# Kernel tuning notes

Measured on AMD Instinct MI355X. Metric: run time of the kernel, lower is better.

The kernel has to match this reference:

```python
import jax, jax.numpy as jnp
import numpy as np
from jax import lax

N = 50000      # nodes
E = 1600000    # edges
F = 128        # input features
G = 32         # gnn_hidden_dim
H = 50         # lstm hidden_dim
SEQ = 10       # sequence_length


def setup_inputs() -> dict:
    key = jax.random.key(0)
    ks = jax.random.split(key, 12)
    s = 0.05
    return {
        "x": jax.random.normal(ks[0], (N, F), jnp.float32),
        "W_gcn": jax.random.normal(ks[1], (F, G), jnp.float32) * s,
        "b_gcn": jnp.zeros((G,), jnp.float32),
        "w_ih0": jax.random.normal(ks[2], (4 * H, G), jnp.float32) * s,
        "w_hh0": jax.random.normal(ks[3], (4 * H, H), jnp.float32) * s,
        "b_ih0": jnp.zeros((4 * H,), jnp.float32),
        "b_hh0": jnp.zeros((4 * H,), jnp.float32),
        "w_ih1": jax.random.normal(ks[4], (4 * H, H), jnp.float32) * s,
        "w_hh1": jax.random.normal(ks[5], (4 * H, H), jnp.float32) * s,
        "b_ih1": jnp.zeros((4 * H,), jnp.float32),
        "b_hh1": jnp.zeros((4 * H,), jnp.float32),
        "fc_w": jax.random.normal(ks[6], (1, H), jnp.float32) * s,
        "fc_b": jnp.zeros((1,), jnp.float32),
        "edge_index": jax.random.randint(ks[7], (2, E), 0, N, dtype=jnp.int64),
        "seq_len": SEQ,
    }


def gcn_conv(x, edge_index, W, b):
    # PyG GCNConv: add self-loops, symmetric deg^{-1/2} normalization,
    # linear transform, gather-scale-scatter aggregation at target nodes.
    n = x.shape[0]
    loop = jnp.arange(n, dtype=edge_index.dtype)
    src = jnp.concatenate([edge_index[0], loop])  # message sources j
    dst = jnp.concatenate([edge_index[1], loop])  # aggregation targets i
    deg = jax.ops.segment_sum(jnp.ones_like(dst, dtype=x.dtype), dst,
                              num_segments=n)
    dinv = jnp.where(deg > 0, lax.rsqrt(jnp.maximum(deg, 1.0)), 0.0)
    norm = dinv[src] * dinv[dst]                       # [E+N]
    h = x @ W                                          # [N, G]
    msg = h[src] * norm[:, None]                       # gather + scale
    out = jax.ops.segment_sum(msg, dst, num_segments=n)
    return out + b


def lstm_layer(x_proj, w_hh, b_hh):
    # x_proj: [T, B, 4H] precomputed input projections (i,f,g,o gate order).
    T, B, H4 = x_proj.shape
    Hd = H4 // 4
    h0 = jnp.zeros((B, Hd), x_proj.dtype)
    c0 = jnp.zeros((B, Hd), x_proj.dtype)

    def step(carry, xp):
        h, c = carry
        gates = xp + h @ w_hh.T + b_hh
        i, f, g, o = jnp.split(gates, 4, axis=-1)
        i, f, o = jax.nn.sigmoid(i), jax.nn.sigmoid(f), jax.nn.sigmoid(o)
        g = jnp.tanh(g)
        c = f * c + i * g
        h = o * jnp.tanh(c)
        return (h, c), h

    (h, c), ys = lax.scan(step, (h0, c0), x_proj)
    return ys, h


def reference(x, W_gcn, b_gcn, w_ih0, w_hh0, b_ih0, b_hh0,
              w_ih1, w_hh1, b_ih1, b_hh1, fc_w, fc_b,
              edge_index, seq_len):
    gnn_out = gcn_conv(x, edge_index, W_gcn, b_gcn)        # [N, G]
    # lstm_in = gnn_out repeated seq_len times -> input projection is
    # identical per step; compute once and broadcast (same math).
    p0 = gnn_out @ w_ih0.T + b_ih0                         # [N, 4H]
    x_proj0 = jnp.broadcast_to(p0, (seq_len,) + p0.shape)  # [T, N, 4H]
    ys0, _ = lstm_layer(x_proj0, w_hh0, b_hh0)             # [T, N, H]
    x_proj1 = ys0 @ w_ih1.T + b_ih1                        # [T, N, 4H]
    _, hn1 = lstm_layer(x_proj1, w_hh1, b_hh1)             # [N, H]
    return hn1 @ fc_w.T + fc_b                             # [N, 1]
```

## Files before the change

kernel.cpp:

```cpp
#include <hip/hip_runtime.h>
#include <hip/hip_bf16.h>

typedef __attribute__((ext_vector_type(8))) short short8;
typedef __attribute__((ext_vector_type(4))) float f32x4;

#define L2E 1.442695041f
#define SCAN_B 256

__device__ __forceinline__ short f2bf(float f) {
  union { __hip_bfloat16 b; short s; } u;
  u.b = __float2bfloat16(f);
  return u.s;
}

__device__ __forceinline__ float ldh(const float* p, size_t i) { return p[i]; }
__device__ __forceinline__ float ldh(const __hip_bfloat16* p, size_t i) {
  return __bfloat162float(p[i]);
}
__device__ __forceinline__ void sth(float* p, size_t i, float v) { p[i] = v; }
__device__ __forceinline__ void sth(__hip_bfloat16* p, size_t i, float v) {
  p[i] = __float2bfloat16(v);
}

__device__ __forceinline__ short8 load_gfrag(const float* g, size_t base) {
  const float4* gp = (const float4*)(g + base);
  float4 a = gp[0], b = gp[1];
  short8 t;
  t[0]=f2bf(a.x); t[1]=f2bf(a.y); t[2]=f2bf(a.z); t[3]=f2bf(a.w);
  t[4]=f2bf(b.x); t[5]=f2bf(b.y); t[6]=f2bf(b.z); t[7]=f2bf(b.w);
  return t;
}
__device__ __forceinline__ short8 load_gfrag(const __hip_bfloat16* g, size_t base) {
  return *(const short8*)(g + base);
}

#define OFF_WIH0 0
#define OFF_WHH0 13312
#define OFF_WIH1 39936
#define OFF_WHH1 66560
#define OFF_B0   93184
#define OFF_B1   94016
#define OFF_FCW  94848
#define IMG_BYTES 95056

__global__ void k_detect(const int* __restrict__ ei, int* __restrict__ flag) {
  if (threadIdx.x == 0 && blockIdx.x == 0) {
    int odd_nz = 0, even_nz = 0;
    for (int i = 0; i < 128; ++i) {
      odd_nz |= (ei[2 * i + 1] != 0);
      even_nz |= (ei[2 * i] != 0);
    }
    *flag = (even_nz && !odd_nz) ? 1 : 0;
  }
}


__global__ void k_count(const int* __restrict__ ei, int E,
                        const int* __restrict__ flag, int* __restrict__ cnt) {
  int e = blockIdx.x * blockDim.x + threadIdx.x;
  if (e < E) {
    int d = (*flag) ? ei[2 * (E + e)] : ei[E + e];
    atomicAdd(&cnt[d], 1);
  }
}

__global__ void k_dinv(const int* __restrict__ cnt, float* __restrict__ dinv, int N) {
  int i = blockIdx.x * blockDim.x + threadIdx.x;
  if (i < N) dinv[i] = rsqrtf((float)cnt[i] + 1.0f);
}

__global__ __launch_bounds__(256) void k_scanA(const int* __restrict__ cnt,
                                               float* __restrict__ dinv,
                                               int* __restrict__ bsum, int N) {
  __shared__ int red[256];
  int b = blockIdx.x, t = threadIdx.x;
  int chunk = (N + SCAN_B - 1) / SCAN_B;
  int lo = b * chunk, hi = min(lo + chunk, N);
  int s = 0;
  for (int i = lo + t; i < hi; i += 256) {
    int c = cnt[i];
    dinv[i] = rsqrtf((float)c + 1.0f);
    s += c;
  }
  red[t] = s;
  __syncthreads();
  for (int o = 128; o > 0; o >>= 1) {
    if (t < o) red[t] += red[t + o];
    __syncthreads();
  }
  if (t == 0) bsum[b] = red[0];
}

__global__ __launch_bounds__(256) void k_scanB(int* __restrict__ a,
                                               const int* __restrict__ bsum,
                                               int N) {
  __shared__ int sh[256];
  int b = blockIdx.x, t = threadIdx.x;
  int chunk = (N + SCAN_B - 1) / SCAN_B;
  int lo = b * chunk, hi = min(lo + chunk, N);
  sh[t] = bsum[t];
  __syncthreads();
  for (int o = 1; o < 256; o <<= 1) {
    int u = (t >= o) ? sh[t - o] : 0;
    __syncthreads();
    sh[t] += u;
    __syncthreads();
  }
  int carry = (b == 0) ? 0 : sh[b - 1];
  __syncthreads();
  for (int i0 = lo; i0 < hi; i0 += 256) {
    int i = i0 + t;
    int c = (i < hi) ? a[i] : 0;
    sh[t] = c;
    __syncthreads();
    for (int o = 1; o < 256; o <<= 1) {
      int u = (t >= o) ? sh[t - o] : 0;
      __syncthreads();
      sh[t] += u;
      __syncthreads();
    }
    if (i < hi) a[i] = carry + sh[t] - c;
    carry += sh[255];
    __syncthreads();
  }
}

template <typename CT>
__global__ void k_fill(const int* __restrict__ ei, int E,
                       const int* __restrict__ flag,
                       int* __restrict__ rowst, CT* __restrict__ csr,
                       int lo, int hi) {
  int e = blockIdx.x * blockDim.x + threadIdx.x;
  if (e < E) {
    int is64 = *flag;
    int d = is64 ? ei[2 * (E + e)] : ei[E + e];
    if (d >= lo && d < hi) {
      int s = is64 ? ei[2 * e] : ei[e];
      int p = atomicAdd(&rowst[d], 1);
      csr[p] = (CT)s;
    }
  }
}

template <typename HT>
__global__ __launch_bounds__(256) void k_hs(const float* __restrict__ x,
                                            const float* __restrict__ Wg,
                                            const float* __restrict__ dinv,
                                            HT* __restrict__ hs, int N) {
  __shared__ __align__(16) float xt[64][132];
  __shared__ __align__(16) float Wl[128][32];
  int tid = threadIdx.x;
  int nb = blockIdx.x * 64;
  for (int i = tid; i < 4096; i += 256) Wl[i >> 5][i & 31] = Wg[i];
  const float4* xv = (const float4*)x;
  for (int i = tid; i < 2048; i += 256) {
    int r = i >> 5, c = i & 31;
    float4 v = make_float4(0.f, 0.f, 0.f, 0.f);
    if (nb + r < N) v = xv[(size_t)(nb + r) * 32 + c];
    *(float4*)&xt[r][c * 4] = v;
  }
  __syncthreads();
  int nl = tid >> 2, gq = (tid & 3) * 8;
  float a[8];
#pragma unroll
  for (int j = 0; j < 8; ++j) a[j] = 0.f;
  for (int k = 0; k < 128; ++k) {
    float xk = xt[nl][k];
#pragma unroll
    for (int j = 0; j < 8; ++j) a[j] += xk * Wl[k][gq + j];
  }
  int n = nb + nl;
  if (n < N) {
    float d = dinv[n];
#pragma unroll
    for (int j = 0; j < 8; ++j) sth(hs, (size_t)n * 32 + gq + j, a[j] * d);
  }
}

template <typename HT, typename GT, typename CT>
__global__ void k_gather(const CT* __restrict__ csr, const int* __restrict__ rowst,
                         const HT* __restrict__ hs, const float* __restrict__ dinv,
                         const float* __restrict__ bg, GT* __restrict__ gout,
                         int N) {
  int w = (blockIdx.x * blockDim.x + threadIdx.x) >> 6;
  if (w >= N) return;
  int l = threadIdx.x & 63;
  int g = l & 31, j = l >> 5;
  int end = rowst[w];
  int start = (w == 0) ? 0 : rowst[w - 1];
  int deg = end - start;
  int dmax = min(deg, 64);
  int idx = (l < deg) ? (int)csr[start + l] : 0;
  float acc = 0.0f;
#pragma unroll 1
  for (int base = 0; base < 64; base += 16) {
    if (base >= dmax) break;
#pragma unroll
    for (int i = 0; i < 8; ++i) {
      int e = base + 2 * i + j;
      int src = __shfl(idx, e);
      float v = ldh(hs, (size_t)src * 32 + g);
      acc += (e < dmax) ? v : 0.0f;
    }
  }
  for (int k = start + 64 + j; k < end; k += 2)
    acc += ldh(hs, (size_t)csr[k] * 32 + g);
  acc += __shfl_xor(acc, 32);
  if (j == 0) {
    float v = (acc + ldh(hs, (size_t)w * 32 + g)) * dinv[w] + bg[g];
    sth(gout, (size_t)w * 32 + g, v);
  }
}

template <typename HT>
__global__ void k_scatter(const int* __restrict__ ei, int E,
                          const int* __restrict__ flag,
                          const HT* __restrict__ hs, float* __restrict__ gout) {
  long long gid = (long long)blockIdx.x * blockDim.x + threadIdx.x;
  int e = (int)(gid >> 3), part = (int)(gid & 7);
  if (e >= E) return;
  int is64 = *flag;
  int s = is64 ? ei[2 * e] : ei[e];
  int d = is64 ? ei[2 * (E + e)] : ei[E + e];
  int b = part * 4;
  float* gp = gout + (size_t)d * 32 + b;
  size_t hp = (size_t)s * 32 + b;
  atomicAdd(gp + 0, ldh(hs, hp + 0));
  atomicAdd(gp + 1, ldh(hs, hp + 1));
  atomicAdd(gp + 2, ldh(hs, hp + 2));
  atomicAdd(gp + 3, ldh(hs, hp + 3));
}
template <typename HT>
__global__ void k_finish(const HT* __restrict__ hs, const float* __restrict__ dinv,
                         const float* __restrict__ bg, float* __restrict__ gout,
                         int N) {
  int gid = blockIdx.x * blockDim.x + threadIdx.x;
  if (gid < N * 32) {
    int n = gid >> 5, g = gid & 31;
    gout[gid] = (gout[gid] + ldh(hs, (size_t)gid)) * dinv[n] + bg[g];
  }
}

__global__ void k_prep(const float* __restrict__ wih0, const float* __restrict__ whh0,
                       const float* __restrict__ wih1, const float* __restrict__ whh1,
                       const float* __restrict__ bih0, const float* __restrict__ bhh0,
                       const float* __restrict__ bih1, const float* __restrict__ bhh1,
                       const float* __restrict__ fcw, unsigned char* __restrict__ img) {
  int gid = blockIdx.x * blockDim.x + threadIdx.x;
  int nthr = gridDim.x * blockDim.x;
  {
    short* W = (short*)(img + OFF_WIH0);
    for (int i = gid; i < 208 * 32; i += nthr) {
      int row = i >> 5, k = i & 31, u = row >> 2, q = row & 3;
      float sc = (q == 2) ? 2.0f * L2E : -L2E;
      float v = (u < 50) ? wih0[(q * 50 + u) * 32 + k] * sc : 0.0f;
      W[row * 32 + (k ^ ((row & 3) << 3))] = f2bf(v);
    }
  }
  {
    short* W = (short*)(img + OFF_WHH0);
    for (int i = gid; i < 208 * 64; i += nthr) {
      int row = i >> 6, k = i & 63, u = row >> 2, q = row & 3;
      float sc = (q == 2) ? 2.0f * L2E : -L2E;
      float v = (u < 50 && k < 50) ? whh0[(q * 50 + u) * 50 + k] * sc : 0.0f;
      W[row * 64 + (k ^ ((row & 7) << 3))] = f2bf(v);
    }
  }
  {
    short* W = (short*)(img + OFF_WIH1);
    for (int i = gid; i < 208 * 64; i += nthr) {
      int row = i >> 6, k = i & 63, u = row >> 2, q = row & 3;
      float sc = (q == 2) ? 2.0f * L2E : -L2E;
      float v = (u < 50 && k < 50) ? wih1[(q * 50 + u) * 50 + k] * sc : 0.0f;
      W[row * 64 + (k ^ ((row & 7) << 3))] = f2bf(v);
    }
  }
  {
    short* W = (short*)(img + OFF_WHH1);
    for (int i = gid; i < 208 * 64; i += nthr) {
      int row = i >> 6, k = i & 63, u = row >> 2, q = row & 3;
      float sc = (q == 2) ? 2.0f * L2E : -L2E;
      float v = (u < 50 && k < 50) ? whh1[(q * 50 + u) * 50 + k] * sc : 0.0f;
      W[row * 64 + (k ^ ((row & 7) << 3))] = f2bf(v);
    }
  }
  {
    float* B = (float*)(img + OFF_B0);
    for (int i = gid; i < 208; i += nthr) {
      int u = i >> 2, q = i & 3;
      float sc = (q == 2) ? 2.0f * L2E : -L2E;
      B[i] = (u < 50) ? (bih0[q * 50 + u] + bhh0[q * 50 + u]) * sc : 0.0f;
    }
  }
  {
    float* B = (float*)(img + OFF_B1);
    for (int i = gid; i < 208; i += nthr) {
      int u = i >> 2, q = i & 3;
      float sc = (q == 2) ? 2.0f * L2E : -L2E;
      B[i] = (u < 50) ? (bih1[q * 50 + u] + bhh1[q * 50 + u]) * sc : 0.0f;
    }
  }
  {
    float* F = (float*)(img + OFF_FCW);
    for (int i = gid; i < 52; i += nthr) F[i] = (i < 50) ? fcw[i] : 0.0f;
  }
}

__device__ __forceinline__ float gate_update(const f32x4& acc, float& cp) {
  float ei = __builtin_amdgcn_exp2f(acc[0]);
  float ef = __builtin_amdgcn_exp2f(acc[1]);
  float eo = __builtin_amdgcn_exp2f(acc[3]);
  float iv = __builtin_amdgcn_rcpf(1.0f + ei);
  float fv = __builtin_amdgcn_rcpf(1.0f + ef);
  float ov = __builtin_amdgcn_rcpf(1.0f + eo);
  float eg = __builtin_amdgcn_exp2f(fminf(acc[2], 80.0f));
  float gv = (eg - 1.0f) * __builtin_amdgcn_rcpf(eg + 1.0f);
  float c = fv * cp + iv * gv;
  cp = c;
  float Ec = __builtin_amdgcn_exp2f(c * (2.0f * L2E));
  float th = (Ec - 1.0f) * __builtin_amdgcn_rcpf(Ec + 1.0f);
  return ov * th;
}

template <typename GT>
__global__ __launch_bounds__(512, 2) void k_lstm(const GT* __restrict__ gout,
    const unsigned char* __restrict__ img, const float* __restrict__ fcb_p,
    float* __restrict__ out, int N) {
  __shared__ __align__(16) unsigned char smem[160592];
  const int tid = threadIdx.x;
  {
    const uint4* s = (const uint4*)img;
    uint4* d = (uint4*)smem;
    for (int i = tid; i < IMG_BYTES / 16; i += 512) d[i] = s[i];
  }
  __syncthreads();
  const int lane = tid & 63, wid = tid >> 6;
  const int l15 = lane & 15, l4 = lane >> 4;
  const int swz7 = (l15 & 7) << 3, swz3 = (l15 & 3) << 3;
  const int node0 = blockIdx.x * 256 + wid * 32;

  const short* WIH0 = (const short*)(smem + OFF_WIH0);
  const short* WHH0 = (const short*)(smem + OFF_WHH0);
  const short* WIH1 = (const short*)(smem + OFF_WIH1);
  const short* WHH1 = (const short*)(smem + OFF_WHH1);
  const float* B0   = (const float*)(smem + OFF_B0);
  const float* B1   = (const float*)(smem + OFF_B1);
  const float* FCW  = (const float*)(smem + OFF_FCW);
  short* h0st = (short*)(smem + IMG_BYTES + wid * 8192);
  short* h1st = h0st + 2048;

  {
    uint4 z; z.x = z.y = z.z = z.w = 0u;
    uint4* p = (uint4*)h0st;
    for (int i = lane; i < 512; i += 64) p[i] = z;
  }

  f32x4 p0r[13][2];
  {
    short8 gfrag[2];
#pragma unroll
    for (int v = 0; v < 2; ++v) {
      int node = node0 + v * 16 + l15;
      short8 t = {0, 0, 0, 0, 0, 0, 0, 0};
      if (node < N) t = load_gfrag(gout, (size_t)node * 32 + l4 * 8);
      gfrag[v] = t;
    }
#pragma unroll
    for (int t = 0; t < 13; ++t) {
      short8 w = *(const short8*)(WIH0 + (16 * t + l15) * 32 + ((l4 * 8) ^ swz3));
      f32x4 bv = *(const f32x4*)(B0 + t * 16 + l4 * 4);
#pragma unroll
      for (int v = 0; v < 2; ++v)
        p0r[t][v] = __builtin_amdgcn_mfma_f32_16x16x32_bf16(w, gfrag[v], bv, 0, 0, 0);
    }
  }

  float c0[13][2], c1[13][2];
#pragma unroll
  for (int t = 0; t < 13; ++t) { c0[t][0]=0.f; c0[t][1]=0.f; c1[t][0]=0.f; c1[t][1]=0.f; }
  float facc[2] = {0.f, 0.f};

#pragma unroll 1
  for (int s = 0; s < 10; ++s) {
    short8 h0f[2][2], h1f[2][2];
#pragma unroll
    for (int c = 0; c < 2; ++c)
#pragma unroll
      for (int v = 0; v < 2; ++v) {
        int nl = v * 16 + l15;
        h0f[c][v] = *(const short8*)(h0st + nl * 64 + ((c * 32 + l4 * 8) ^ swz7));
        h1f[c][v] = *(const short8*)(h1st + nl * 64 + ((c * 32 + l4 * 8) ^ swz7));
      }
#pragma unroll
    for (int t = 0; t < 13; ++t) {
      int arow = (16 * t + l15);
      short8 ah0 = *(const short8*)(WHH0 + arow * 64 + ((l4 * 8) ^ swz7));
      short8 ah1 = *(const short8*)(WHH0 + arow * 64 + ((32 + l4 * 8) ^ swz7));
#pragma unroll
      for (int v = 0; v < 2; ++v) {
        f32x4 acc = p0r[t][v];
        acc = __builtin_amdgcn_mfma_f32_16x16x32_bf16(ah0, h0f[0][v], acc, 0, 0, 0);
        acc = __builtin_amdgcn_mfma_f32_16x16x32_bf16(ah1, h0f[1][v], acc, 0, 0, 0);
        float h = gate_update(acc, c0[t][v]);
        h0st[(v * 16 + l15) * 64 + ((4 * t + l4) ^ swz7)] = f2bf(h);
      }
    }
    short8 h0nf[2][2];
#pragma unroll
    for (int c = 0; c < 2; ++c)
#pragma unroll
      for (int v = 0; v < 2; ++v) {
        int nl = v * 16 + l15;
        h0nf[c][v] = *(const short8*)(h0st + nl * 64 + ((c * 32 + l4 * 8) ^ swz7));
      }
#pragma unroll
    for (int t = 0; t < 13; ++t) {
      f32x4 bv = *(const f32x4*)(B1 + t * 16 + l4 * 4);
      int arow = (16 * t + l15);
      short8 ai0 = *(const short8*)(WIH1 + arow * 64 + ((l4 * 8) ^ swz7));
      short8 ai1 = *(const short8*)(WIH1 + arow * 64 + ((32 + l4 * 8) ^ swz7));
      short8 ah0 = *(const short8*)(WHH1 + arow * 64 + ((l4 * 8) ^ swz7));
      short8 ah1 = *(const short8*)(WHH1 + arow * 64 + ((32 + l4 * 8) ^ swz7));
#pragma unroll
      for (int v = 0; v < 2; ++v) {
        f32x4 acc = bv;
        acc = __builtin_amdgcn_mfma_f32_16x16x32_bf16(ai0, h0nf[0][v], acc, 0, 0, 0);
        acc = __builtin_amdgcn_mfma_f32_16x16x32_bf16(ai1, h0nf[1][v], acc, 0, 0, 0);
        acc = __builtin_amdgcn_mfma_f32_16x16x32_bf16(ah0, h1f[0][v], acc, 0, 0, 0);
        acc = __builtin_amdgcn_mfma_f32_16x16x32_bf16(ah1, h1f[1][v], acc, 0, 0, 0);
        float h = gate_update(acc, c1[t][v]);
        h1st[(v * 16 + l15) * 64 + ((4 * t + l4) ^ swz7)] = f2bf(h);
        if (s == 9) {
          int u = 4 * t + l4;
          facc[v] += FCW[u] * h;
        }
      }
    }
  }
  float fcb = fcb_p[0];
#pragma unroll
  for (int v = 0; v < 2; ++v) {
    float r = facc[v];
    r += __shfl_xor(r, 16);
    r += __shfl_xor(r, 32);
    int node = node0 + v * 16 + l15;
    if (l4 == 0 && node < N) out[node] = r + fcb;
  }
}

extern "C" void kernel_launch(void* const* d_in, const int* in_sizes, int n_in,
                              void* d_out, int out_size, void* d_ws, size_t ws_size,
                              hipStream_t stream) {
  const float* x    = (const float*)d_in[0];
  const float* Wg   = (const float*)d_in[1];
  const float* bg   = (const float*)d_in[2];
  const float* wih0 = (const float*)d_in[3];
  const float* whh0 = (const float*)d_in[4];
  const float* bih0 = (const float*)d_in[5];
  const float* bhh0 = (const float*)d_in[6];
  const float* wih1 = (const float*)d_in[7];
  const float* whh1 = (const float*)d_in[8];
  const float* bih1 = (const float*)d_in[9];
  const float* bhh1 = (const float*)d_in[10];
  const float* fcw  = (const float*)d_in[11];
  const float* fcb  = (const float*)d_in[12];
  const int*   edge = (const int*)d_in[13];
  int N = in_sizes[0] / 128;
  int E = in_sizes[13] / 2;

  char* ws = (char*)d_ws;
  size_t off = 0;
  auto take = [&](size_t b) {
    size_t o = off;
    off = (off + b + 255) & ~(size_t)255;
    return o;
  };
  int*   rowst = (int*)(ws + take((size_t)N * 4));
  float* dinv  = (float*)(ws + take((size_t)N * 4));
  int*   flag  = (int*)(ws + take(256));
  int*   bsum  = (int*)(ws + take(SCAN_B * 4));
  unsigned char* wimg = (unsigned char*)(ws + take(IMG_BYTES));

  size_t base = off;
  size_t needA = base + (((size_t)N * 128 + 255) & ~(size_t)255)
               + (((size_t)E * 4 + 255) & ~(size_t)255)
               + ((size_t)N * 128);
  size_t needB = base + (((size_t)N * 64 + 255) & ~(size_t)255)
               + (((size_t)E * 2 + 255) & ~(size_t)255)
               + ((size_t)N * 64);
  bool canU16 = (N <= 65535);

  const int NP = 8;
  int span = (N + NP - 1) / NP;

  hipMemsetAsync(rowst, 0, (size_t)N * 4, stream);
  k_detect<<<1, 1, 0, stream>>>(edge, flag);
  k_count<<<(E + 255) / 256, 256, 0, stream>>>(edge, E, flag, rowst);
  k_prep<<<52, 256, 0, stream>>>(wih0, whh0, wih1, whh1, bih0, bhh0, bih1, bhh1,
                                 fcw, wimg);

  if (ws_size >= needA) {
    float* gout = (float*)(ws + take((size_t)N * 128));
    int*   csr  = (int*)(ws + take((size_t)E * 4));
    float* hs   = (float*)(ws + take((size_t)N * 128));
    k_scanA<<<SCAN_B, 256, 0, stream>>>(rowst, dinv, bsum, N);
    k_scanB<<<SCAN_B, 256, 0, stream>>>(rowst, bsum, N);
    k_hs<float><<<(N + 63) / 64, 256, 0, stream>>>(x, Wg, dinv, hs, N);
    for (int p = 0; p < NP; ++p) {
      int lo = p * span, hi = min(lo + span, N);
      if (lo >= hi) break;
      k_fill<int><<<(E + 255) / 256, 256, 0, stream>>>(edge, E, flag, rowst,
                                                       csr, lo, hi);
    }
    k_gather<float, float, int><<<(N + 3) / 4, 256, 0, stream>>>(
        csr, rowst, hs, dinv, bg, gout, N);
    k_lstm<float><<<(N + 255) / 256, 512, 0, stream>>>(gout, wimg, fcb,
                                                       (float*)d_out, N);
  } else if (canU16 && ws_size >= needB) {
    __hip_bfloat16* gout = (__hip_bfloat16*)(ws + take((size_t)N * 64));
    unsigned short* csr  = (unsigned short*)(ws + take((size_t)E * 2));
    __hip_bfloat16* hs   = (__hip_bfloat16*)(ws + take((size_t)N * 64));
    k_scanA<<<SCAN_B, 256, 0, stream>>>(rowst, dinv, bsum, N);
    k_scanB<<<SCAN_B, 256, 0, stream>>>(rowst, bsum, N);
    k_hs<__hip_bfloat16><<<(N + 63) / 64, 256, 0, stream>>>(x, Wg, dinv, hs, N);
    for (int p = 0; p < NP; ++p) {
      int lo = p * span, hi = min(lo + span, N);
      if (lo >= hi) break;
      k_fill<unsigned short><<<(E + 255) / 256, 256, 0, stream>>>(
          edge, E, flag, rowst, csr, lo, hi);
    }
    k_gather<__hip_bfloat16, __hip_bfloat16, unsigned short>
        <<<(N + 3) / 4, 256, 0, stream>>>(csr, rowst, hs, dinv, bg, gout, N);
    k_lstm<__hip_bfloat16><<<(N + 255) / 256, 512, 0, stream>>>(gout, wimg, fcb,
                                                                (float*)d_out, N);
  } else {
    float* gout = (float*)(ws + take((size_t)N * 128));
    __hip_bfloat16* hs = (__hip_bfloat16*)(ws + take((size_t)N * 64));
    hipMemsetAsync(gout, 0, (size_t)N * 128, stream);
    k_dinv<<<(N + 255) / 256, 256, 0, stream>>>(rowst, dinv, N);
    k_hs<__hip_bfloat16><<<(N + 63) / 64, 256, 0, stream>>>(x, Wg, dinv, hs, N);
    int sc_blocks = (int)(((long long)E * 8 + 255) / 256);
    k_scatter<__hip_bfloat16><<<sc_blocks, 256, 0, stream>>>(edge, E, flag, hs, gout);
    k_finish<__hip_bfloat16><<<(N * 32 + 255) / 256, 256, 0, stream>>>(
        hs, dinv, bg, gout, N);
    k_lstm<float><<<(N + 255) / 256, 512, 0, stream>>>(gout, wimg, fcb,
                                                       (float*)d_out, N);
  }
}
```

Baseline: 350.5 us.

## Pack edges into compact 32-bit words once and reuse across fill passes

In the 16-bit CSR path, a new conversion kernel reads the int64/int32 edge list once. It packs src and dst into one 32-bit word and counts degrees in the same pass, replacing the separate count kernel. The partitioned CSR fill passes then read only the packed 4-byte words instead of re-reading the wide edge index, and the number of passes drops from 8 to 4. Workspace buffers are aliased (packed edges share space with hs/gout, bsum with csr) so this path fits in a smaller workspace. Fewer passes mean more scattered atomics per pass, and the path only applies when the larger fp32 path is not chosen.

New measurement: 343.7 us. No clear change (-1.9%).

```diff
diff --git a/kernel.cpp b/kernel.cpp
--- a/kernel.cpp
+++ b/kernel.cpp
@@ -60,6 +60,19 @@
   int e = blockIdx.x * blockDim.x + threadIdx.x;
   if (e < E) {
     int d = (*flag) ? ei[2 * (E + e)] : ei[E + e];
+    atomicAdd(&cnt[d], 1);
+  }
+}
+
+__global__ void k_convert(const int* __restrict__ ei, int E,
+                          const int* __restrict__ flag,
+                          unsigned int* __restrict__ ed, int* __restrict__ cnt) {
+  int e = blockIdx.x * blockDim.x + threadIdx.x;
+  if (e < E) {
+    int is64 = *flag;
+    int s = is64 ? ei[2 * e] : ei[e];
+    int d = is64 ? ei[2 * (E + e)] : ei[E + e];
+    ed[e] = (unsigned int)s | ((unsigned int)d << 16);
     atomicAdd(&cnt[d], 1);
   }
 }
@@ -122,6 +135,20 @@
     if (i < hi) a[i] = carry + sh[t] - c;
     carry += sh[255];
     __syncthreads();
+  }
+}
+
+__global__ void k_fill_p(const unsigned int* __restrict__ ed, int E,
+                         int* __restrict__ rowst,
+                         unsigned short* __restrict__ csr, int lo, int hi) {
+  int e = blockIdx.x * blockDim.x + threadIdx.x;
+  if (e < E) {
+    unsigned int v = ed[e];
+    int d = (int)(v >> 16);
+    if (d >= lo && d < hi) {
+      int p = atomicAdd(&rowst[d], 1);
+      csr[p] = (unsigned short)(v & 0xFFFFu);
+    }
   }
 }
 
@@ -478,24 +505,23 @@
   int*   rowst = (int*)(ws + take((size_t)N * 4));
   float* dinv  = (float*)(ws + take((size_t)N * 4));
   int*   flag  = (int*)(ws + take(256));
-  int*   bsum  = (int*)(ws + take(SCAN_B * 4));
   unsigned char* wimg = (unsigned char*)(ws + take(IMG_BYTES));
-
   size_t base = off;
+
+  const int NP = 4;
+  int span = (N + NP - 1) / NP;
+  bool canU16 = (N <= 65535) && (E <= 100000000);
+
+  size_t csr_b  = ((size_t)E * 2 + 255) & ~(size_t)255;
+  size_t hsb    = ((size_t)N * 64 + 255) & ~(size_t)255;
+  size_t reg2_b = (size_t)E * 4 > 2 * hsb ? (size_t)E * 4 : 2 * hsb;
+  size_t needP  = base + csr_b + reg2_b;
   size_t needA = base + (((size_t)N * 128 + 255) & ~(size_t)255)
                + (((size_t)E * 4 + 255) & ~(size_t)255)
                + ((size_t)N * 128);
-  size_t needB = base + (((size_t)N * 64 + 255) & ~(size_t)255)
-               + (((size_t)E * 2 + 255) & ~(size_t)255)
-               + ((size_t)N * 64);
-  bool canU16 = (N <= 65535);
-
-  const int NP = 8;
-  int span = (N + NP - 1) / NP;
 
   hipMemsetAsync(rowst, 0, (size_t)N * 4, stream);
   k_detect<<<1, 1, 0, stream>>>(edge, flag);
-  k_count<<<(E + 255) / 256, 256, 0, stream>>>(edge, E, flag, rowst);
   k_prep<<<52, 256, 0, stream>>>(wih0, whh0, wih1, whh1, bih0, bhh0, bih1, bhh1,
                                  fcw, wimg);
 
@@ -503,6 +529,8 @@
     float* gout = (float*)(ws + take((size_t)N * 128));
     int*   csr  = (int*)(ws + take((size_t)E * 4));
     float* hs   = (float*)(ws + take((size_t)N * 128));
+    int*   bsum = (int*)csr;
+    k_count<<<(E + 255) / 256, 256, 0, stream>>>(edge, E, flag, rowst);
     k_scanA<<<SCAN_B, 256, 0, stream>>>(rowst, dinv, bsum, N);
     k_scanB<<<SCAN_B, 256, 0, stream>>>(rowst, bsum, N);
     k_hs<float><<<(N + 63) / 64, 256, 0, stream>>>(x, Wg, dinv, hs, N);
@@ -516,19 +544,23 @@
         csr, rowst, hs, dinv, bg, gout, N);
     k_lstm<float><<<(N + 255) / 256, 512, 0, stream>>>(gout, wimg, fcb,
                                                        (float*)d_out, N);
-  } else if (canU16 && ws_size >= needB) {
-    __hip_bfloat16* gout = (__hip_bfloat16*)(ws + take((size_t)N * 64));
-    unsigned short* csr  = (unsigned short*)(ws + take((size_t)E * 2));
-    __hip_bfloat16* hs   = (__hip_bfloat16*)(ws + take((size_t)N * 64));
+  } else if (canU16 && ws_size >= needP) {
+    unsigned short* csr = (unsigned short*)(ws + take(csr_b));
+    char* reg2 = ws + take(reg2_b);
+    unsigned int*   ed   = (unsigned int*)reg2;
+    __hip_bfloat16* hs   = (__hip_bfloat16*)reg2;
+    __hip_bfloat16* gout = (__hip_bfloat16*)(reg2 + hsb);
+    int* bsum = (int*)csr;
+
+    k_convert<<<(E + 255) / 256, 256, 0, stream>>>(edge, E, flag, ed, rowst);
     k_scanA<<<SCAN_B, 256, 0, stream>>>(rowst, dinv, bsum, N);
     k_scanB<<<SCAN_B, 256, 0, stream>>>(rowst, bsum, N);
-    k_hs<__hip_bfloat16><<<(N + 63) / 64, 256, 0, stream>>>(x, Wg, dinv, hs, N);
     for (int p = 0; p < NP; ++p) {
       int lo = p * span, hi = min(lo + span, N);
       if (lo >= hi) break;
-      k_fill<unsigned short><<<(E + 255) / 256, 256, 0, stream>>>(
-          edge, E, flag, rowst, csr, lo, hi);
-    }
+      k_fill_p<<<(E + 255) / 256, 256, 0, stream>>>(ed, E, rowst, csr, lo, hi);
+    }
+    k_hs<__hip_bfloat16><<<(N + 63) / 64, 256, 0, stream>>>(x, Wg, dinv, hs, N);
     k_gather<__hip_bfloat16, __hip_bfloat16, unsigned short>
         <<<(N + 3) / 4, 256, 0, stream>>>(csr, rowst, hs, dinv, bg, gout, N);
     k_lstm<__hip_bfloat16><<<(N + 255) / 256, 512, 0, stream>>>(gout, wimg, fcb,
@@ -537,6 +569,7 @@
     float* gout = (float*)(ws + take((size_t)N * 128));
     __hip_bfloat16* hs = (__hip_bfloat16*)(ws + take((size_t)N * 64));
     hipMemsetAsync(gout, 0, (size_t)N * 128, stream);
+    k_count<<<(E + 255) / 256, 256, 0, stream>>>(edge, E, flag, rowst);
     k_dinv<<<(N + 255) / 256, 256, 0, stream>>>(rowst, dinv, N);
     k_hs<__hip_bfloat16><<<(N + 63) / 64, 256, 0, stream>>>(x, Wg, dinv, hs, N);
     int sc_blocks = (int)(((long long)E * 8 + 255) / 256);
```
